# Kernel optimization log

Hardware: AMD Instinct MI355X
Metric: run time of the kernel (lower is better)

Reference implementation:

```python
import jax, jax.numpy as jnp
import numpy as np

H = 1024          # hidden_size
NH = 16           # num_attention_heads
HD = H // NH      # attention_head_size = 64
B, S = 8, 1024
LN_EPS = 1e-12


def setup_inputs() -> dict:
    key = jax.random.key(0)
    ks = jax.random.split(key, 12)
    sc = 0.02
    return {
        "input_tensor": jax.random.normal(ks[0], (B, S, H), dtype=jnp.float32),
        "attention_mask": jnp.zeros((B, S), dtype=jnp.float32),
        # LinearMem params (quantization disabled -> plain Linear, torch layout [out,in])
        "Wq": jax.random.normal(ks[1], (H, H), dtype=jnp.float32) * sc,
        "bq": jnp.zeros((H,), dtype=jnp.float32),
        "Wk": jax.random.normal(ks[2], (H, H), dtype=jnp.float32) * sc,
        "bk": jnp.zeros((H,), dtype=jnp.float32),
        "Wv": jax.random.normal(ks[3], (H, H), dtype=jnp.float32) * sc,
        "bv": jnp.zeros((H,), dtype=jnp.float32),
        "Wo": jax.random.normal(ks[4], (H, H), dtype=jnp.float32) * sc,
        "bo": jnp.zeros((H,), dtype=jnp.float32),
        "ln_gamma": jnp.ones((H,), dtype=jnp.float32),
        "ln_beta": jnp.zeros((H,), dtype=jnp.float32),
    }


def _heads(x):  # [B,S,H] -> [B,NH,S,HD]
    return x.reshape(B, S, NH, HD).transpose(0, 2, 1, 3)


def reference(input_tensor, attention_mask, Wq, bq, Wk, bk, Wv, bv, Wo, bo, ln_gamma, ln_beta):
    # Q/K/V projections (LinearMem with quantization disabled == Linear)
    q = _heads(jnp.einsum('bsh,oh->bso', input_tensor, Wq) + bq)
    k = _heads(jnp.einsum('bsh,oh->bso', input_tensor, Wk) + bk)
    v = _heads(jnp.einsum('bsh,oh->bso', input_tensor, Wv) + bv)
    scores = jnp.einsum('bnqd,bnkd->bnqk', q, k) / np.float32(np.sqrt(HD))
    scores = scores + attention_mask[:, None, None, :]  # additive mask [B,1,1,S]
    probs = jax.nn.softmax(scores, axis=-1)  # dropout = identity in eval
    ctx = jnp.einsum('bnqk,bnkd->bnqd', probs, v)
    ctx = ctx.transpose(0, 2, 1, 3).reshape(B, S, H)
    # output projection + residual LayerNorm (eps=1e-12)
    out = jnp.einsum('bsh,oh->bso', ctx, Wo) + bo
    resid = out + input_tensor
    mu = jnp.mean(resid, axis=-1, keepdims=True)
    var = jnp.mean(jnp.square(resid - mu), axis=-1, keepdims=True)
    return (resid - mu) * jax.lax.rsqrt(var + LN_EPS) * ln_gamma + ln_beta
```

## Files before the change

### kernel.cpp

```cpp
#include <hip/hip_runtime.h>

#define NHh 16

typedef unsigned short ushortT;
typedef __attribute__((ext_vector_type(8))) short short8;
typedef __attribute__((ext_vector_type(4))) float floatx4;

__device__ __forceinline__ ushortT f2bf(float x) {
    union { float f; unsigned int u; } cv; cv.f = x;
    unsigned int u = cv.u;
    unsigned int r = u + 0x7fffu + ((u >> 16) & 1u);
    return (ushortT)(r >> 16);
}

__device__ __forceinline__ unsigned pack2_trunc(float a, float b) {
    union { float f; unsigned u; } ua, ub;
    ua.f = a; ub.f = b;
    return (ub.u & 0xffff0000u) | (ua.u >> 16);
}

__device__ __forceinline__ void gload_lds16(const ushortT* g, ushortT* l) {
    __builtin_amdgcn_global_load_lds(
        (const __attribute__((address_space(1))) void*)g,
        (__attribute__((address_space(3))) void*)l, 16, 0, 0);
}

__global__ __launch_bounds__(256) void cvt_x(const float* __restrict__ in,
                                             ushortT* __restrict__ out, int n4) {
    int i = blockIdx.x * 256 + threadIdx.x;
    if (i >= n4) return;
    float4 f = ((const float4*)in)[i];
    uint2 o;
    o.x = (unsigned)f2bf(f.x) | ((unsigned)f2bf(f.y) << 16);
    o.y = (unsigned)f2bf(f.z) | ((unsigned)f2bf(f.w) << 16);
    ((uint2*)out)[i] = o;
}

__global__ __launch_bounds__(256) void cvt_w(const float* __restrict__ W0, const float* __restrict__ W1,
                                             const float* __restrict__ W2, const float* __restrict__ W3,
                                             ushortT* __restrict__ o0, ushortT* __restrict__ o1,
                                             ushortT* __restrict__ o2, ushortT* __restrict__ o3, int n4) {
    int z = blockIdx.y;
    const float* in = (z == 0) ? W0 : (z == 1) ? W1 : (z == 2) ? W2 : W3;
    ushortT* out = (z == 0) ? o0 : (z == 1) ? o1 : (z == 2) ? o2 : o3;
    int i = blockIdx.x * 256 + threadIdx.x;
    if (i >= n4) return;
    float4 f = ((const float4*)in)[i];
    uint2 o;
    o.x = (unsigned)f2bf(f.x) | ((unsigned)f2bf(f.y) << 16);
    o.y = (unsigned)f2bf(f.z) | ((unsigned)f2bf(f.w) << 16);
    ((uint2*)out)[i] = o;
}

__global__ __launch_bounds__(256) void qkv_gemm(const ushortT* __restrict__ X,
        const ushortT* __restrict__ W0, const ushortT* __restrict__ W1, const ushortT* __restrict__ W2,
        const float* __restrict__ b0, const float* __restrict__ b1, const float* __restrict__ b2,
        ushortT* __restrict__ Qo, ushortT* __restrict__ Ko, ushortT* __restrict__ Vo) {
    __shared__ ushortT As[128 * 32];
    __shared__ ushortT Bs[128 * 32];
    const int l = blockIdx.x;
    const int mt = l & 63;
    const int r = l >> 6;
    const int z = r >> 3;
    const int nt = r & 7;
    const int tid = threadIdx.x;
    const int lane = tid & 63;
    const int w = tid >> 6;
    const int qd = lane >> 4;
    const int ln = lane & 15;
    const ushortT* Wt = (z == 0) ? W0 : (z == 1) ? W1 : W2;
    const float* bias = (z == 0) ? b0 : (z == 1) ? b1 : b2;
    const int RM = (w >> 1) * 64;
    const int RN = (w & 1) * 64;

    const ushortT* Ap;
    const ushortT* Bp;
    int arow0, brow0;
    if (z == 2) { Ap = Wt; arow0 = nt * 128; Bp = X;  brow0 = mt * 128; }
    else        { Ap = X;  arow0 = mt * 128; Bp = Wt; brow0 = nt * 128; }

    floatx4 acc[4][4];
#pragma unroll
    for (int i = 0; i < 4; i++)
#pragma unroll
        for (int j = 0; j < 4; j++) acc[i][j] = (floatx4){0.f, 0.f, 0.f, 0.f};

    const int c0 = tid, c1 = tid + 256;
    for (int k0 = 0; k0 < 1024; k0 += 32) {
        gload_lds16(Ap + (size_t)(arow0 + (c0 >> 2)) * 1024 + k0 + (c0 & 3) * 8, As + c0 * 8);
        gload_lds16(Ap + (size_t)(arow0 + (c1 >> 2)) * 1024 + k0 + (c1 & 3) * 8, As + c1 * 8);
        gload_lds16(Bp + (size_t)(brow0 + (c0 >> 2)) * 1024 + k0 + (c0 & 3) * 8, Bs + c0 * 8);
        gload_lds16(Bp + (size_t)(brow0 + (c1 >> 2)) * 1024 + k0 + (c1 & 3) * 8, Bs + c1 * 8);
        __syncthreads();
        short8 af[4], bf8[4];
#pragma unroll
        for (int i = 0; i < 4; i++) af[i] = *(const short8*)&As[(RM + i * 16 + ln) * 32 + qd * 8];
#pragma unroll
        for (int j = 0; j < 4; j++) bf8[j] = *(const short8*)&Bs[(RN + j * 16 + ln) * 32 + qd * 8];
#pragma unroll
        for (int i = 0; i < 4; i++)
#pragma unroll
            for (int j = 0; j < 4; j++)
                acc[i][j] = __builtin_amdgcn_mfma_f32_16x16x32_bf16(af[i], bf8[j], acc[i][j], 0, 0, 0);
        __syncthreads();
    }

    if (z == 2) {
        floatx4 bias4[4];
#pragma unroll
        for (int i = 0; i < 4; i++) bias4[i] = *(const floatx4*)(bias + arow0 + RM + i * 16 + qd * 4);
#pragma unroll
        for (int j = 0; j < 4; j++) {
            int m = brow0 + RN + j * 16 + ln;
            int bb = m >> 10, s = m & 1023;
#pragma unroll
            for (int i = 0; i < 4; i++) {
#pragma unroll
                for (int r2 = 0; r2 < 4; r2++) {
                    int a = arow0 + RM + i * 16 + qd * 4 + r2;
                    int hh = a >> 6, dd = a & 63;
                    float v = acc[i][j][r2] + bias4[i][r2];
                    Vo[((size_t)(bb * NHh + hh) * 64 + dd) * 1024 + s] = f2bf(v);
                }
            }
        }
    } else {
        ushortT* Out = (z == 0) ? Qo : Ko;
#pragma unroll
        for (int j = 0; j < 4; j++) {
            int n = brow0 + RN + j * 16 + ln;
            float bb = bias[n];
            int h = n >> 6, d = n & 63;
#pragma unroll
            for (int i = 0; i < 4; i++) {
#pragma unroll
                for (int r2 = 0; r2 < 4; r2++) {
                    int m = arow0 + RM + i * 16 + qd * 4 + r2;
                    int b = m >> 10, s = m & 1023;
                    float v = acc[i][j][r2] + bb;
                    Out[(size_t)((b * NHh + h) * 1024 + s) * 64 + d] = f2bf(v);
                }
            }
        }
    }
}

__global__ __launch_bounds__(256) void oproj_gemm(const ushortT* __restrict__ A,
        const ushortT* __restrict__ Wt, const float* __restrict__ bias, float* __restrict__ Pj) {
    __shared__ ushortT As[128 * 32];
    __shared__ ushortT Bs[128 * 32];
    const int l = blockIdx.x;
    const int m0 = (l & 63) * 128;
    const int n0 = (l >> 6) * 128;
    const int tid = threadIdx.x;
    const int lane = tid & 63;
    const int w = tid >> 6;
    const int qd = lane >> 4;
    const int ln = lane & 15;
    const int RM = (w >> 1) * 64;
    const int RN = (w & 1) * 64;

    floatx4 acc[4][4];
#pragma unroll
    for (int i = 0; i < 4; i++)
#pragma unroll
        for (int j = 0; j < 4; j++) acc[i][j] = (floatx4){0.f, 0.f, 0.f, 0.f};

    const int c0 = tid, c1 = tid + 256;
    for (int k0 = 0; k0 < 1024; k0 += 32) {
        gload_lds16(A + (size_t)(m0 + (c0 >> 2)) * 1024 + k0 + (c0 & 3) * 8, As + c0 * 8);
        gload_lds16(A + (size_t)(m0 + (c1 >> 2)) * 1024 + k0 + (c1 & 3) * 8, As + c1 * 8);
        gload_lds16(Wt + (size_t)(n0 + (c0 >> 2)) * 1024 + k0 + (c0 & 3) * 8, Bs + c0 * 8);
        gload_lds16(Wt + (size_t)(n0 + (c1 >> 2)) * 1024 + k0 + (c1 & 3) * 8, Bs + c1 * 8);
        __syncthreads();
        short8 af[4], bf8[4];
#pragma unroll
        for (int i = 0; i < 4; i++) af[i] = *(const short8*)&As[(RM + i * 16 + ln) * 32 + qd * 8];
#pragma unroll
        for (int j = 0; j < 4; j++) bf8[j] = *(const short8*)&Bs[(RN + j * 16 + ln) * 32 + qd * 8];
#pragma unroll
        for (int i = 0; i < 4; i++)
#pragma unroll
            for (int j = 0; j < 4; j++)
                acc[i][j] = __builtin_amdgcn_mfma_f32_16x16x32_bf16(af[i], bf8[j], acc[i][j], 0, 0, 0);
        __syncthreads();
    }

#pragma unroll
    for (int j = 0; j < 4; j++) {
        int n = n0 + RN + j * 16 + ln;
        float bb = bias[n];
#pragma unroll
        for (int i = 0; i < 4; i++) {
#pragma unroll
            for (int r2 = 0; r2 < 4; r2++) {
                int m = m0 + RM + i * 16 + qd * 4 + r2;
                Pj[(size_t)m * 1024 + n] = acc[i][j][r2] + bb;
            }
        }
    }
}

__global__ __launch_bounds__(256, 2) void attn_kernel(const ushortT* __restrict__ Q,
        const ushortT* __restrict__ K, const ushortT* __restrict__ Vg_t,
        const float* __restrict__ mask, ushortT* __restrict__ ctx) {
    __shared__ __align__(16) ushortT Ks[128 * 64];
    __shared__ __align__(16) ushortT Vt[64 * 128];
    __shared__ __align__(16) ushortT Ps[4][64 * 72];

    const int tid = threadIdx.x;
    const int lane = tid & 63;
    const int w = tid >> 6;
    const int qd = lane >> 4;
    const int ln = lane & 15;
    const int l = blockIdx.x;
    const int bh = l & 127;
    const int b = bh >> 4;
    const int h = bh & 15;
    const int qb = l >> 7;

    const ushortT* Qg = Q + (size_t)bh * 65536;
    const ushortT* Kg = K + (size_t)bh * 65536;
    const ushortT* Vg = Vg_t + (size_t)bh * 65536;
    const float* mrow = mask + b * 1024;
    const float LOG2E = 1.4426950408889634f;
    const float SCL = 0.125f * 1.4426950408889634f;

    short8 qf[4][2];
#pragma unroll
    for (int nj = 0; nj < 4; nj++)
#pragma unroll
        for (int ks = 0; ks < 2; ks++)
            qf[nj][ks] = *(const short8*)(Qg + (size_t)(qb * 256 + w * 64 + nj * 16 + ln) * 64 + ks * 32 + qd * 8);

    float lst[4] = {0.f, 0.f, 0.f, 0.f};
    floatx4 accO[4][4];
#pragma unroll
    for (int i = 0; i < 4; i++)
#pragma unroll
        for (int j = 0; j < 4; j++) accO[i][j] = (floatx4){0.f, 0.f, 0.f, 0.f};

    const int ksr = lane >> 3;
    const int kc  = lane & 7;
    const int vdr = lane >> 4;
    const int vcc = lane & 15;

    for (int kt = 0; kt < 8; ++kt) {
        __syncthreads();

#pragma unroll
        for (int ii = 0; ii < 4; ii++) {
            int i = w * 4 + ii;
            int srow = i * 8 + ksr;
            gload_lds16(Kg + (size_t)(kt * 128 + srow) * 64 + (kc ^ ksr) * 8,
                        Ks + i * 512 + lane * 8);
        }
#pragma unroll
        for (int ii = 0; ii < 4; ii++) {
            int i = w * 4 + ii;
            int d = i * 4 + vdr;
            gload_lds16(Vg + (size_t)d * 1024 + kt * 128 + (vcc ^ (d & 15)) * 8,
                        Vt + i * 512 + lane * 8);
        }

        __syncthreads();

#pragma unroll
        for (int h2 = 0; h2 < 2; ++h2) {
            const int s0g = kt * 128 + h2 * 64;

#pragma unroll
            for (int njp = 0; njp < 2; ++njp) {
                floatx4 sv[4][2];
#pragma unroll
                for (int mi = 0; mi < 4; mi++)
#pragma unroll
                    for (int j = 0; j < 2; j++) sv[mi][j] = (floatx4){0.f, 0.f, 0.f, 0.f};
#pragma unroll
                for (int ks = 0; ks < 2; ks++) {
                    short8 af[4];
#pragma unroll
                    for (int mi = 0; mi < 4; mi++)
                        af[mi] = *(const short8*)&Ks[(h2 * 64 + mi * 16 + ln) * 64 +
                                                     (((ks * 4 + qd) ^ (ln & 7)) * 8)];
#pragma unroll
                    for (int mi = 0; mi < 4; mi++)
#pragma unroll
                        for (int j = 0; j < 2; j++)
                            sv[mi][j] = __builtin_amdgcn_mfma_f32_16x16x32_bf16(af[mi], qf[njp * 2 + j][ks], sv[mi][j], 0, 0, 0);
                }

                float rs0 = 0.f, rs1 = 0.f;
#pragma unroll
                for (int mi = 0; mi < 4; mi++) {
                    floatx4 m4 = *(const floatx4*)(mrow + s0g + mi * 16 + qd * 4);
                    float p00 = __builtin_amdgcn_exp2f(sv[mi][0][0] * SCL + m4[0] * LOG2E);
                    float p01 = __builtin_amdgcn_exp2f(sv[mi][0][1] * SCL + m4[1] * LOG2E);
                    float p02 = __builtin_amdgcn_exp2f(sv[mi][0][2] * SCL + m4[2] * LOG2E);
                    float p03 = __builtin_amdgcn_exp2f(sv[mi][0][3] * SCL + m4[3] * LOG2E);
                    float p10 = __builtin_amdgcn_exp2f(sv[mi][1][0] * SCL + m4[0] * LOG2E);
                    float p11 = __builtin_amdgcn_exp2f(sv[mi][1][1] * SCL + m4[1] * LOG2E);
                    float p12 = __builtin_amdgcn_exp2f(sv[mi][1][2] * SCL + m4[2] * LOG2E);
                    float p13 = __builtin_amdgcn_exp2f(sv[mi][1][3] * SCL + m4[3] * LOG2E);
                    rs0 += (p00 + p01) + (p02 + p03);
                    rs1 += (p10 + p11) + (p12 + p13);
                    uint2 w0, w1;
                    w0.x = pack2_trunc(p00, p01); w0.y = pack2_trunc(p02, p03);
                    w1.x = pack2_trunc(p10, p11); w1.y = pack2_trunc(p12, p13);
                    *(uint2*)&Ps[w][(njp * 32 + ln) * 72 + mi * 16 + qd * 4] = w0;
                    *(uint2*)&Ps[w][(njp * 32 + 16 + ln) * 72 + mi * 16 + qd * 4] = w1;
                }
                rs0 += __shfl_xor(rs0, 16, 64); rs0 += __shfl_xor(rs0, 32, 64);
                rs1 += __shfl_xor(rs1, 16, 64); rs1 += __shfl_xor(rs1, 32, 64);
                lst[njp * 2 + 0] += rs0;
                lst[njp * 2 + 1] += rs1;
            }

#pragma unroll
            for (int ks2 = 0; ks2 < 2; ks2++) {
                short8 ap[4], bv[4];
#pragma unroll
                for (int i = 0; i < 4; i++)
                    ap[i] = *(const short8*)&Ps[w][(i * 16 + ln) * 72 + ks2 * 32 + qd * 8];
#pragma unroll
                for (int j = 0; j < 4; j++)
                    bv[j] = *(const short8*)&Vt[(j * 16 + ln) * 128 +
                                                (((h2 * 8 + ks2 * 4 + qd) ^ ln) * 8)];
#pragma unroll
                for (int i = 0; i < 4; i++)
#pragma unroll
                    for (int j = 0; j < 4; j++)
                        accO[i][j] = __builtin_amdgcn_mfma_f32_16x16x32_bf16(ap[i], bv[j], accO[i][j], 0, 0, 0);
            }
        }
    }

#pragma unroll
    for (int i = 0; i < 4; i++) {
#pragma unroll
        for (int r = 0; r < 4; r++) {
            float lv = __shfl(lst[i], qd * 4 + r, 64);
            float linv = 1.f / lv;
            int q = qb * 256 + w * 64 + i * 16 + qd * 4 + r;
#pragma unroll
            for (int j = 0; j < 4; j++) {
                int d = j * 16 + ln;
                ctx[((size_t)(b * 1024 + q)) * 1024 + h * 64 + d] = f2bf(accO[i][j][r] * linv);
            }
        }
    }
}

__global__ __launch_bounds__(256) void ln_kernel(const float* __restrict__ Pj, const float* __restrict__ X,
        const float* __restrict__ gamma, const float* __restrict__ beta, float* __restrict__ out) {
    __shared__ float red[8];
    int row = blockIdx.x;
    int t = threadIdx.x;
    const float4 p4 = ((const float4*)(Pj + (size_t)row * 1024))[t];
    const float4 x4 = ((const float4*)(X + (size_t)row * 1024))[t];
    float r0 = p4.x + x4.x, r1 = p4.y + x4.y, r2 = p4.z + x4.z, r3 = p4.w + x4.w;
    float s = r0 + r1 + r2 + r3;
    float ss = r0 * r0 + r1 * r1 + r2 * r2 + r3 * r3;
#pragma unroll
    for (int o = 1; o < 64; o <<= 1) { s += __shfl_xor(s, o, 64); ss += __shfl_xor(ss, o, 64); }
    int w = t >> 6;
    if ((t & 63) == 0) { red[w] = s; red[4 + w] = ss; }
    __syncthreads();
    s = red[0] + red[1] + red[2] + red[3];
    ss = red[4] + red[5] + red[6] + red[7];
    float mu = s * (1.f / 1024.f);
    float var = ss * (1.f / 1024.f) - mu * mu;
    float inv = rsqrtf(var + 1e-12f);
    const float4 g4 = ((const float4*)gamma)[t];
    const float4 b4 = ((const float4*)beta)[t];
    float4 o4;
    o4.x = (r0 - mu) * inv * g4.x + b4.x;
    o4.y = (r1 - mu) * inv * g4.y + b4.y;
    o4.z = (r2 - mu) * inv * g4.z + b4.z;
    o4.w = (r3 - mu) * inv * g4.w + b4.w;
    ((float4*)(out + (size_t)row * 1024))[t] = o4;
}

extern "C" void kernel_launch(void* const* d_in, const int* in_sizes, int n_in,
                              void* d_out, int out_size, void* d_ws, size_t ws_size,
                              hipStream_t stream) {
    const float* x     = (const float*)d_in[0];
    const float* mask  = (const float*)d_in[1];
    const float* Wq    = (const float*)d_in[2];
    const float* bq    = (const float*)d_in[3];
    const float* Wk    = (const float*)d_in[4];
    const float* bk    = (const float*)d_in[5];
    const float* Wv    = (const float*)d_in[6];
    const float* bv    = (const float*)d_in[7];
    const float* Wo    = (const float*)d_in[8];
    const float* bo    = (const float*)d_in[9];
    const float* gamma = (const float*)d_in[10];
    const float* beta  = (const float*)d_in[11];
    float* out = (float*)d_out;

    char* ws = (char*)d_ws;
    ushortT* Xb  = (ushortT*)(ws);
    ushortT* Wqb = (ushortT*)(ws + (16u << 20));
    ushortT* Wkb = (ushortT*)(ws + (18u << 20));
    ushortT* Wvb = (ushortT*)(ws + (20u << 20));
    ushortT* Wob = (ushortT*)(ws + (22u << 20));
    ushortT* Qb  = (ushortT*)(ws + (24u << 20));
    ushortT* Kb  = (ushortT*)(ws + (40u << 20));
    ushortT* Vb  = (ushortT*)(ws + (56u << 20));
    ushortT* Cb  = (ushortT*)(ws);
    float*   Pj  = (float*)(ws + (24u << 20));

    cvt_x<<<8192, 256, 0, stream>>>(x, Xb, 2097152);
    cvt_w<<<dim3(1024, 4), 256, 0, stream>>>(Wq, Wk, Wv, Wo, Wqb, Wkb, Wvb, Wob, 262144);
    qkv_gemm<<<1536, 256, 0, stream>>>(Xb, Wqb, Wkb, Wvb, bq, bk, bv, Qb, Kb, Vb);
    attn_kernel<<<512, 256, 0, stream>>>(Qb, Kb, Vb, mask, Cb);
    oproj_gemm<<<512, 256, 0, stream>>>(Cb, Wob, bo, Pj);
    ln_kernel<<<8192, 256, 0, stream>>>(Pj, x, gamma, beta, out);
}
```

Measured before the change: 291.3 us.

## Rewrite QKV GEMM as 256x256-tile double-buffered pipelined kernel with swizzled LDS

Replaces the 128x128, single-buffered QKV projection GEMM with a 512-thread kernel that computes 256x256 output tiles using a K-step of 64. Global-to-LDS loads are double-buffered and issued in quarter-tile stages interleaved with MFMA phases, with explicit vmcnt waits and raised wave priority during MFMA. The LDS layout uses an XOR swizzle to avoid bank conflicts. The aim is to hide load latency and improve operand reuse. The cost is more registers and LDS per block and only 384 blocks, which may leave some CUs with uneven load.

```diff
diff --git a/kernel.cpp b/kernel.cpp
--- a/kernel.cpp
+++ b/kernel.cpp
@@ -52,93 +52,147 @@
     ((uint2*)out)[i] = o;
 }
 
-__global__ __launch_bounds__(256) void qkv_gemm(const ushortT* __restrict__ X,
+__device__ __forceinline__ short8 lds_frag(const ushortT* tb, int row, int ks, int qd) {
+    int rowblk = row >> 4;
+    int r = row & 15;
+    int c2 = qd ^ ((r >> 3) << 1);
+    return *(const short8*)((const char*)tb + rowblk * 2048 + ks * 1024 + r * 64 + c2 * 16);
+}
+
+__global__ __launch_bounds__(512, 2) void qkv256(
+        const ushortT* __restrict__ X,
         const ushortT* __restrict__ W0, const ushortT* __restrict__ W1, const ushortT* __restrict__ W2,
         const float* __restrict__ b0, const float* __restrict__ b1, const float* __restrict__ b2,
         ushortT* __restrict__ Qo, ushortT* __restrict__ Ko, ushortT* __restrict__ Vo) {
-    __shared__ ushortT As[128 * 32];
-    __shared__ ushortT Bs[128 * 32];
+    __shared__ __align__(16) ushortT As[2 * 16384];
+    __shared__ __align__(16) ushortT Bs[2 * 16384];
+
     const int l = blockIdx.x;
-    const int mt = l & 63;
-    const int r = l >> 6;
-    const int z = r >> 3;
-    const int nt = r & 7;
+    const int z = l >> 7;
+    const int idx = l & 127;
     const int tid = threadIdx.x;
     const int lane = tid & 63;
     const int w = tid >> 6;
+    const int wr = w >> 2;
+    const int wc = w & 3;
     const int qd = lane >> 4;
     const int ln = lane & 15;
-    const ushortT* Wt = (z == 0) ? W0 : (z == 1) ? W1 : W2;
-    const float* bias = (z == 0) ? b0 : (z == 1) ? b1 : b2;
-    const int RM = (w >> 1) * 64;
-    const int RN = (w & 1) * 64;
-
-    const ushortT* Ap;
-    const ushortT* Bp;
+
+    const ushortT* Ap; const ushortT* Bp;
     int arow0, brow0;
-    if (z == 2) { Ap = Wt; arow0 = nt * 128; Bp = X;  brow0 = mt * 128; }
-    else        { Ap = X;  arow0 = mt * 128; Bp = Wt; brow0 = nt * 128; }
-
-    floatx4 acc[4][4];
-#pragma unroll
-    for (int i = 0; i < 4; i++)
+    if (z == 2) { Ap = W2; arow0 = (idx & 3) * 256; Bp = X; brow0 = (idx >> 2) * 256; }
+    else { Ap = X; arow0 = (idx >> 2) * 256; Bp = (z == 0) ? W0 : W1; brow0 = (idx & 3) * 256; }
+
+    floatx4 acc[8][4];
+#pragma unroll
+    for (int i = 0; i < 8; i++)
 #pragma unroll
         for (int j = 0; j < 4; j++) acc[i][j] = (floatx4){0.f, 0.f, 0.f, 0.f};
 
-    const int c0 = tid, c1 = tid + 256;
-    for (int k0 = 0; k0 < 1024; k0 += 32) {
-        gload_lds16(Ap + (size_t)(arow0 + (c0 >> 2)) * 1024 + k0 + (c0 & 3) * 8, As + c0 * 8);
-        gload_lds16(Ap + (size_t)(arow0 + (c1 >> 2)) * 1024 + k0 + (c1 & 3) * 8, As + c1 * 8);
-        gload_lds16(Bp + (size_t)(brow0 + (c0 >> 2)) * 1024 + k0 + (c0 & 3) * 8, Bs + c0 * 8);
-        gload_lds16(Bp + (size_t)(brow0 + (c1 >> 2)) * 1024 + k0 + (c1 & 3) * 8, Bs + c1 * 8);
-        __syncthreads();
-        short8 af[4], bf8[4];
-#pragma unroll
-        for (int i = 0; i < 4; i++) af[i] = *(const short8*)&As[(RM + i * 16 + ln) * 32 + qd * 8];
-#pragma unroll
-        for (int j = 0; j < 4; j++) bf8[j] = *(const short8*)&Bs[(RN + j * 16 + ln) * 32 + qd * 8];
-#pragma unroll
-        for (int i = 0; i < 4; i++)
-#pragma unroll
-            for (int j = 0; j < 4; j++)
-                acc[i][j] = __builtin_amdgcn_mfma_f32_16x16x32_bf16(af[i], bf8[j], acc[i][j], 0, 0, 0);
-        __syncthreads();
+    auto STAGE = [&](int cursor) {
+        int kt = cursor >> 2;
+        if (kt >= 16) return;
+        int h = cursor & 3;
+        int buf = kt & 1;
+        int k0 = kt << 6;
+        const ushortT* G = (h < 2) ? Ap : Bp;
+        int row0 = (h < 2) ? arow0 : brow0;
+        ushortT* L = (h < 2) ? (As + buf * 16384) : (Bs + buf * 16384);
+        int half = h & 1;
+#pragma unroll
+        for (int j = 0; j < 2; j++) {
+            int o = half * 16384 + j * 8192 + tid * 16;
+            int rowblk = o >> 11;
+            int colblk = (o >> 10) & 1;
+            int r = (o >> 6) & 15;
+            int c2 = ((o >> 4) & 3) ^ ((r >> 3) << 1);
+            gload_lds16(G + (size_t)(row0 + rowblk * 16 + r) * 1024 + k0 + colblk * 32 + c2 * 8,
+                        (ushortT*)((char*)L + o));
+        }
+    };
+
+    for (int c = 0; c < 7; c++) STAGE(c);
+    asm volatile("s_waitcnt vmcnt(6)" ::: "memory");
+    __builtin_amdgcn_s_barrier();
+
+    short8 afr[4][2], bfr[2][2];
+    int cursor = 7;
+    for (int T = 0; T < 16; T++) {
+        const ushortT* Ab = As + (T & 1) * 16384;
+        const ushortT* Bb = Bs + (T & 1) * 16384;
+#pragma unroll
+        for (int ph = 0; ph < 4; ph++) {
+            const int mq = ph >> 1, nq = ph & 1;
+#pragma unroll
+            for (int ni = 0; ni < 2; ni++)
+#pragma unroll
+                for (int ks = 0; ks < 2; ks++)
+                    bfr[ni][ks] = lds_frag(Bb, nq * 128 + ni * 64 + wc * 16 + ln, ks, qd);
+            if (nq == 0) {
+#pragma unroll
+                for (int mi = 0; mi < 4; mi++)
+#pragma unroll
+                    for (int ks = 0; ks < 2; ks++)
+                        afr[mi][ks] = lds_frag(Ab, (mq * 4 + mi) * 32 + wr * 16 + ln, ks, qd);
+            }
+            STAGE(cursor); ++cursor;
+            __builtin_amdgcn_s_barrier();
+            asm volatile("s_waitcnt lgkmcnt(0)" ::: "memory");
+            __builtin_amdgcn_s_setprio(1);
+#pragma unroll
+            for (int mi = 0; mi < 4; mi++)
+#pragma unroll
+                for (int ni = 0; ni < 2; ni++)
+#pragma unroll
+                    for (int ks = 0; ks < 2; ks++)
+                        acc[mq * 4 + mi][nq * 2 + ni] =
+                            __builtin_amdgcn_mfma_f32_16x16x32_bf16(afr[mi][ks], bfr[ni][ks],
+                                                                    acc[mq * 4 + mi][nq * 2 + ni], 0, 0, 0);
+            __builtin_amdgcn_s_setprio(0);
+            if (ph == 3) {
+                if (T < 14) { asm volatile("s_waitcnt vmcnt(6)" ::: "memory"); }
+                else        { asm volatile("s_waitcnt vmcnt(0)" ::: "memory"); }
+            }
+            __builtin_amdgcn_s_barrier();
+        }
     }
 
     if (z == 2) {
-        floatx4 bias4[4];
-#pragma unroll
-        for (int i = 0; i < 4; i++) bias4[i] = *(const floatx4*)(bias + arow0 + RM + i * 16 + qd * 4);
-#pragma unroll
-        for (int j = 0; j < 4; j++) {
-            int m = brow0 + RN + j * 16 + ln;
-            int bb = m >> 10, s = m & 1023;
-#pragma unroll
-            for (int i = 0; i < 4; i++) {
+        floatx4 bv4[8];
+#pragma unroll
+        for (int mi = 0; mi < 8; mi++)
+            bv4[mi] = *(const floatx4*)(b2 + arow0 + mi * 32 + wr * 16 + qd * 4);
+#pragma unroll
+        for (int ni = 0; ni < 4; ni++) {
+            int n = brow0 + ni * 64 + wc * 16 + ln;
+            int bb = n >> 10, s = n & 1023;
+#pragma unroll
+            for (int mi = 0; mi < 8; mi++) {
 #pragma unroll
                 for (int r2 = 0; r2 < 4; r2++) {
-                    int a = arow0 + RM + i * 16 + qd * 4 + r2;
-                    int hh = a >> 6, dd = a & 63;
-                    float v = acc[i][j][r2] + bias4[i][r2];
-                    Vo[((size_t)(bb * NHh + hh) * 64 + dd) * 1024 + s] = f2bf(v);
+                    int dim = arow0 + mi * 32 + wr * 16 + qd * 4 + r2;
+                    int hh = dim >> 6, dd = dim & 63;
+                    Vo[((size_t)(bb * NHh + hh) * 64 + dd) * 1024 + s] =
+                        f2bf(acc[mi][ni][r2] + bv4[mi][r2]);
                 }
             }
         }
     } else {
-        ushortT* Out = (z == 0) ? Qo : Ko;
-#pragma unroll
-        for (int j = 0; j < 4; j++) {
-            int n = brow0 + RN + j * 16 + ln;
+        ushortT* Out = z ? Ko : Qo;
+        const float* bias = z ? b1 : b0;
+#pragma unroll
+        for (int ni = 0; ni < 4; ni++) {
+            int n = brow0 + ni * 64 + wc * 16 + ln;
             float bb = bias[n];
             int h = n >> 6, d = n & 63;
 #pragma unroll
-            for (int i = 0; i < 4; i++) {
+            for (int mi = 0; mi < 8; mi++) {
 #pragma unroll
                 for (int r2 = 0; r2 < 4; r2++) {
-                    int m = arow0 + RM + i * 16 + qd * 4 + r2;
+                    int m = arow0 + mi * 32 + wr * 16 + qd * 4 + r2;
                     int b = m >> 10, s = m & 1023;
-                    float v = acc[i][j][r2] + bb;
-                    Out[(size_t)((b * NHh + h) * 1024 + s) * 64 + d] = f2bf(v);
+                    Out[(size_t)((b * NHh + h) * 1024 + s) * 64 + d] =
+                        f2bf(acc[mi][ni][r2] + bb);
                 }
             }
         }
@@ -412,7 +466,7 @@
 
     cvt_x<<<8192, 256, 0, stream>>>(x, Xb, 2097152);
     cvt_w<<<dim3(1024, 4), 256, 0, stream>>>(Wq, Wk, Wv, Wo, Wqb, Wkb, Wvb, Wob, 262144);
-    qkv_gemm<<<1536, 256, 0, stream>>>(Xb, Wqb, Wkb, Wvb, bq, bk, bv, Qb, Kb, Vb);
+    qkv256<<<384, 512, 0, stream>>>(Xb, Wqb, Wkb, Wvb, bq, bk, bv, Qb, Kb, Vb);
     attn_kernel<<<512, 256, 0, stream>>>(Qb, Kb, Vb, mask, Cb);
     oproj_gemm<<<512, 256, 0, stream>>>(Cb, Wob, bo, Pj);
     ln_kernel<<<8192, 256, 0, stream>>>(Pj, x, gamma, beta, out);
```

After: 292.5 us. About the same (+0.4%).
